# Optimization experiments

Hardware: AMD Instinct MI355X
Metric: run time of the kernel (lower is better)

Reference implementation:

```python
import jax, jax.numpy as jnp
import numpy as np

N = 100000          # nodes
E = 1600000         # edges (before self-loops)
IN = 128
H, C = 4, 32        # heads, out_channels per head
EPS = 1e-5          # BatchNorm eps
NEG_SLOPE = 0.2     # GATConv LeakyReLU slope


def setup_inputs() -> dict:
    key = jax.random.key(0)
    ks = jax.random.split(key, 8)
    return {
        "x": jax.random.normal(ks[0], (N, IN), jnp.float32),
        "edge_index": jax.random.randint(ks[1], (2, E), 0, N, dtype=jnp.int64),
        "W": jax.random.normal(ks[2], (IN, H * C), jnp.float32) * (1.0 / np.sqrt(IN)),
        "att_src": jax.random.normal(ks[3], (H, C), jnp.float32) * 0.1,
        "att_dst": jax.random.normal(ks[4], (H, C), jnp.float32) * 0.1,
        "bias": jax.random.normal(ks[5], (H * C,), jnp.float32) * 0.01,
        "gamma": jnp.ones((H * C,), jnp.float32),
        "beta": jnp.zeros((H * C,), jnp.float32),
    }


def reference(x, edge_index, W, att_src, att_dst, bias, gamma, beta):
    # --- GATConv (concat heads, add self-loops, eval-mode dropout) ---
    loop = jnp.arange(N, dtype=edge_index.dtype)
    src = jnp.concatenate([edge_index[0], loop])  # [E+N] message sources
    dst = jnp.concatenate([edge_index[1], loop])  # [E+N] message targets

    h = (x @ W).reshape(N, H, C)                       # [N,H,C]
    a_s = jnp.einsum('nhc,hc->nh', h, att_src)          # [N,H]
    a_d = jnp.einsum('nhc,hc->nh', h, att_dst)          # [N,H]

    e = a_s[src] + a_d[dst]                             # [E+N,H]
    e = jnp.where(e > 0, e, NEG_SLOPE * e)              # LeakyReLU

    # segment softmax over incoming edges of each dst node
    m = jax.ops.segment_max(e, dst, num_segments=N)     # [N,H]
    ex = jnp.exp(e - m[dst])
    den = jax.ops.segment_sum(ex, dst, num_segments=N)  # [N,H]
    alpha = ex / den[dst]                               # [E+N,H]

    out = jax.ops.segment_sum(h[src] * alpha[:, :, None], dst, num_segments=N)
    out = out.reshape(N, H * C) + bias                  # [N,128]

    # --- ELU activation ---
    out = jax.nn.elu(out)

    # --- BatchNorm1d (training-mode batch statistics, biased variance) ---
    mean = out.mean(axis=0)
    var = out.var(axis=0)
    return (out - mean) * jax.lax.rsqrt(var + EPS) * gamma + beta
```

## Files before the change

### kernel.cpp

```cpp
#include <hip/hip_runtime.h>

#define NEG 0.2f
#define MAXD 128
#define NR 8
#define GEMM_BLOCKS 1024
#define COUNT_BLOCKS 2048

__device__ __forceinline__ float lrelu(float v) { return v > 0.f ? v : NEG * v; }

__device__ __forceinline__ unsigned f2bf(float f) {
  unsigned u = __float_as_uint(f);
  u = (u + 0x7FFFu + ((u >> 16) & 1u)) >> 16;
  return u;
}
__device__ __forceinline__ float bf_lo(unsigned u) { return __uint_as_float(u << 16); }
__device__ __forceinline__ float bf_hi(unsigned u) { return __uint_as_float(u & 0xFFFF0000u); }

typedef __attribute__((ext_vector_type(8))) short bf16x8;
typedef __attribute__((ext_vector_type(4))) float f32x4;

__global__ __launch_bounds__(256) void k_prep(const float* __restrict__ W,
                                              const float* __restrict__ att_src,
                                              const float* __restrict__ att_dst,
                                              unsigned short* __restrict__ Bext) {
  for (int id = blockIdx.x * 256 + threadIdx.x; id < 9 * 4 * 64 * 8; id += gridDim.x * 256) {
    int j = id & 7, lane = (id >> 3) & 63, kb = (id >> 9) & 3, ct = id >> 11;
    int k = kb * 32 + (lane >> 4) * 8 + j;
    int c = ct * 16 + (lane & 15);
    float v;
    if (c < 128) {
      v = W[k * 128 + c];
    } else {
      int slot = c - 128;
      int hd = slot & 3;
      const float* att = (slot < 4) ? att_src : att_dst;
      float s = 0.f;
      for (int jj = 0; jj < 32; ++jj) s = fmaf(W[k * 128 + hd * 32 + jj], att[hd * 32 + jj], s);
      v = s;
    }
    Bext[id] = (unsigned short)f2bf(v);
  }
}

__global__ __launch_bounds__(256) void k_gemm_count(
    const float* __restrict__ x, const unsigned short* __restrict__ Bext,
    unsigned* __restrict__ hb, float* __restrict__ a_s, float* __restrict__ a_d,
    int N, int ntiles,
    const int* __restrict__ ei, int* __restrict__ cnt, int* __restrict__ rank,
    int E, int rsize)
{
  const int tid = threadIdx.x;
  const int chunk = blockIdx.x >> 3;
  if (chunk % 3 == 0) {
    const int vb = (chunk / 3) * 8 + (blockIdx.x & 7);
    const bf16x8* Bfrag = reinterpret_cast<const bf16x8*>(Bext);
    const int w = tid >> 6, lane = tid & 63;
    const int r16 = lane & 15, g = lane >> 4;
    for (int tile = vb; tile < ntiles; tile += GEMM_BLOCKS) {
      int n0 = tile * 64 + w * 16;
      int rowc = min(n0 + r16, N - 1);
      const float* xp = x + (size_t)rowc * 128 + g * 8;
      bf16x8 afr[4];
#pragma unroll
      for (int kb = 0; kb < 4; ++kb) {
        float4 lo = *reinterpret_cast<const float4*>(xp + kb * 32);
        float4 hi = *reinterpret_cast<const float4*>(xp + kb * 32 + 4);
        bf16x8 t;
        t[0] = (short)f2bf(lo.x); t[1] = (short)f2bf(lo.y);
        t[2] = (short)f2bf(lo.z); t[3] = (short)f2bf(lo.w);
        t[4] = (short)f2bf(hi.x); t[5] = (short)f2bf(hi.y);
        t[6] = (short)f2bf(hi.z); t[7] = (short)f2bf(hi.w);
        afr[kb] = t;
      }
#pragma unroll
      for (int ct = 0; ct < 9; ++ct) {
        f32x4 acc = {0.f, 0.f, 0.f, 0.f};
#pragma unroll
        for (int kb = 0; kb < 4; ++kb) {
          bf16x8 bfr = Bfrag[(ct * 4 + kb) * 64 + lane];
          acc = __builtin_amdgcn_mfma_f32_16x16x32_bf16(afr[kb], bfr, acc, 0, 0, 0);
        }
        if (ct < 8) {
#pragma unroll
          for (int r = 0; r < 4; ++r) {
            int orow = n0 + g * 4 + r;
            unsigned b = f2bf(acc[r]);
            unsigned partner = __shfl_xor(b, 1);
            if (((lane & 1) == 0) && orow < N)
              hb[(size_t)orow * 64 + ct * 8 + (r16 >> 1)] = b | (partner << 16);
          }
        } else {
#pragma unroll
          for (int r = 0; r < 4; ++r) {
            int orow = n0 + g * 4 + r;
            if (r16 < 8 && orow < N) {
              if (r16 < 4) a_s[orow * 4 + r16] = acc[r];
              else         a_d[orow * 4 + (r16 - 4)] = acc[r];
            }
          }
        }
      }
    }
  } else {
    const int r = blockIdx.x & 7;
    const int lo = r * rsize, hi = lo + rsize;
    const int cidx = chunk - 1 - (chunk / 3);
    const int gtid = cidx * 256 + tid;
    const int gstride = (COUNT_BLOCKS >> 3) * 256;
    const int nquad = E >> 2;
    const int4* dst4 = reinterpret_cast<const int4*>(ei + E);
    for (int q = gtid; q < nquad; q += gstride) {
      int4 d = dst4[q];
      int e0 = q << 2;
      if (d.x >= lo && d.x < hi) rank[e0]     = atomicAdd(&cnt[d.x], 1);
      if (d.y >= lo && d.y < hi) rank[e0 + 1] = atomicAdd(&cnt[d.y], 1);
      if (d.z >= lo && d.z < hi) rank[e0 + 2] = atomicAdd(&cnt[d.z], 1);
      if (d.w >= lo && d.w < hi) rank[e0 + 3] = atomicAdd(&cnt[d.w], 1);
    }
    for (int e = (nquad << 2) + gtid; e < E; e += gstride) {
      int d = ei[E + e];
      if (d >= lo && d < hi) rank[e] = atomicAdd(&cnt[d], 1);
    }
  }
}

__global__ __launch_bounds__(256) void k_scan1(const int* __restrict__ cnt, int* __restrict__ incl,
                                               int* __restrict__ bsum, int N) {
  __shared__ int sm[256];
  int i = blockIdx.x * 256 + threadIdx.x;
  int v = (i < N) ? cnt[i] : 0;
  sm[threadIdx.x] = v;
  __syncthreads();
  for (int off = 1; off < 256; off <<= 1) {
    int t = (threadIdx.x >= off) ? sm[threadIdx.x - off] : 0;
    __syncthreads();
    sm[threadIdx.x] += t;
    __syncthreads();
  }
  if (i < N) incl[i] = sm[threadIdx.x];
  if (threadIdx.x == 255) bsum[blockIdx.x] = sm[255];
}

__global__ __launch_bounds__(512) void k_scan2(int* __restrict__ bsum, int nb) {
  __shared__ int sm[512];
  int v = (threadIdx.x < nb) ? bsum[threadIdx.x] : 0;
  sm[threadIdx.x] = v;
  __syncthreads();
  for (int off = 1; off < 512; off <<= 1) {
    int t = (threadIdx.x >= off) ? sm[threadIdx.x - off] : 0;
    __syncthreads();
    sm[threadIdx.x] += t;
    __syncthreads();
  }
  if (threadIdx.x < nb) bsum[threadIdx.x] = sm[threadIdx.x];
}

__global__ __launch_bounds__(256) void k_scan3(const int* __restrict__ cnt, const int* __restrict__ incl,
                                               const int* __restrict__ bsum, int* __restrict__ offs,
                                               int N, int E) {
  int i = blockIdx.x * 256 + threadIdx.x;
  if (i < N) {
    int base = (blockIdx.x > 0) ? bsum[blockIdx.x - 1] : 0;
    offs[i] = base + incl[i] - cnt[i];
  }
  if (i == 0) offs[N] = E;
}

__global__ __launch_bounds__(256) void k_scatter_rank(const int* __restrict__ ei,
                                                      const int* __restrict__ offs,
                                                      const int* __restrict__ rank,
                                                      int* __restrict__ ssrc, int E, int rsize) {
  const int r = blockIdx.x & 7;
  const int lo = r * rsize, hi = lo + rsize;
  const int gtid = (blockIdx.x >> 3) * 256 + threadIdx.x;
  const int gstride = (gridDim.x >> 3) * 256;
  const int nquad = E >> 2;
  const int4* dst4 = reinterpret_cast<const int4*>(ei + E);
  for (int q = gtid; q < nquad; q += gstride) {
    int4 d = dst4[q];
    int e0 = q << 2;
    if (d.x >= lo && d.x < hi) ssrc[offs[d.x] + rank[e0]]     = ei[e0];
    if (d.y >= lo && d.y < hi) ssrc[offs[d.y] + rank[e0 + 1]] = ei[e0 + 1];
    if (d.z >= lo && d.z < hi) ssrc[offs[d.z] + rank[e0 + 2]] = ei[e0 + 2];
    if (d.w >= lo && d.w < hi) ssrc[offs[d.w] + rank[e0 + 3]] = ei[e0 + 3];
  }
  for (int e = (nquad << 2) + gtid; e < E; e += gstride) {
    int d = ei[E + e];
    if (d >= lo && d < hi) ssrc[offs[d] + rank[e]] = ei[e];
  }
}

__global__ __launch_bounds__(256) void k_agg(
    const unsigned* __restrict__ hb, const float* __restrict__ a_s, const float* __restrict__ a_d,
    const int* __restrict__ offs, const int* __restrict__ ssrc,
    const float* __restrict__ bias, unsigned* __restrict__ preb,
    float* __restrict__ bnpart, int N)
{
  __shared__ float al[4][MAXD][4];
  __shared__ int   ls[4][MAXD];
  __shared__ float sv[4][128];
  const int wv = threadIdx.x >> 6;
  const int lane = threadIdx.x & 63;
  const int n = blockIdx.x * 4 + wv;

  if (n < N) {
    const int hsel = lane >> 4;
    const int start = offs[n], end = offs[n + 1];
    const int deg = end - start;
    const int jm = deg < MAXD ? deg : MAXD;
    float4 adv = *reinterpret_cast<const float4*>(&a_d[n * 4]);
    float4 asv = *reinterpret_cast<const float4*>(&a_s[n * 4]);
    float e0 = __expf(lrelu(asv.x + adv.x));
    float e1 = __expf(lrelu(asv.y + adv.y));
    float e2 = __expf(lrelu(asv.z + adv.z));
    float e3 = __expf(lrelu(asv.w + adv.w));
    float p0 = 0.f, p1 = 0.f, p2 = 0.f, p3 = 0.f;
    for (int j = lane; j < deg; j += 64) {
      int s = ssrc[start + j];
      float4 av = *reinterpret_cast<const float4*>(&a_s[s * 4]);
      float x0 = __expf(lrelu(av.x + adv.x));
      float x1 = __expf(lrelu(av.y + adv.y));
      float x2 = __expf(lrelu(av.z + adv.z));
      float x3 = __expf(lrelu(av.w + adv.w));
      p0 += x0; p1 += x1; p2 += x2; p3 += x3;
      if (j < MAXD) {
        float4 t = make_float4(x0, x1, x2, x3);
        *reinterpret_cast<float4*>(&al[wv][j][0]) = t;
        ls[wv][j] = s;
      }
    }
#pragma unroll
    for (int off = 32; off >= 1; off >>= 1) {
      p0 += __shfl_xor(p0, off);
      p1 += __shfl_xor(p1, off);
      p2 += __shfl_xor(p2, off);
      p3 += __shfl_xor(p3, off);
    }
    float rden0 = 1.f / (p0 + e0), rden1 = 1.f / (p1 + e1);
    float rden2 = 1.f / (p2 + e2), rden3 = 1.f / (p3 + e3);
    for (int j = lane; j < jm; j += 64) {
      float4 t = *reinterpret_cast<float4*>(&al[wv][j][0]);
      t.x *= rden0; t.y *= rden1; t.z *= rden2; t.w *= rden3;
      *reinterpret_cast<float4*>(&al[wv][j][0]) = t;
    }
    float ad_c = (hsel < 2) ? (hsel == 0 ? adv.x : adv.y) : (hsel == 2 ? adv.z : adv.w);
    float rden = (hsel < 2) ? (hsel == 0 ? rden0 : rden1) : (hsel == 2 ? rden2 : rden3);
    float esf = (hsel < 2) ? (hsel == 0 ? e0 : e1) : (hsel == 2 ? e2 : e3);
    unsigned us = hb[(size_t)n * 64 + lane];
    float wself = esf * rden;
    float acc0 = wself * bf_lo(us);
    float acc1 = wself * bf_hi(us);
    int j = 0;
    for (; j + 8 <= jm; j += 8) {
      int4 sA = *reinterpret_cast<int4*>(&ls[wv][j]);
      int4 sB = *reinterpret_cast<int4*>(&ls[wv][j + 4]);
      unsigned u0 = hb[(size_t)sA.x * 64 + lane];
      unsigned u1 = hb[(size_t)sA.y * 64 + lane];
      unsigned u2 = hb[(size_t)sA.z * 64 + lane];
      unsigned u3 = hb[(size_t)sA.w * 64 + lane];
      unsigned u4 = hb[(size_t)sB.x * 64 + lane];
      unsigned u5 = hb[(size_t)sB.y * 64 + lane];
      unsigned u6 = hb[(size_t)sB.z * 64 + lane];
      unsigned u7 = hb[(size_t)sB.w * 64 + lane];
      float w0 = al[wv][j][hsel];
      float w1 = al[wv][j + 1][hsel];
      float w2 = al[wv][j + 2][hsel];
      float w3 = al[wv][j + 3][hsel];
      float w4 = al[wv][j + 4][hsel];
      float w5 = al[wv][j + 5][hsel];
      float w6 = al[wv][j + 6][hsel];
      float w7 = al[wv][j + 7][hsel];
      acc0 = fmaf(w0, bf_lo(u0), acc0);
      acc1 = fmaf(w0, bf_hi(u0), acc1);
      acc0 = fmaf(w1, bf_lo(u1), acc0);
      acc1 = fmaf(w1, bf_hi(u1), acc1);
      acc0 = fmaf(w2, bf_lo(u2), acc0);
      acc1 = fmaf(w2, bf_hi(u2), acc1);
      acc0 = fmaf(w3, bf_lo(u3), acc0);
      acc1 = fmaf(w3, bf_hi(u3), acc1);
      acc0 = fmaf(w4, bf_lo(u4), acc0);
      acc1 = fmaf(w4, bf_hi(u4), acc1);
      acc0 = fmaf(w5, bf_lo(u5), acc0);
      acc1 = fmaf(w5, bf_hi(u5), acc1);
      acc0 = fmaf(w6, bf_lo(u6), acc0);
      acc1 = fmaf(w6, bf_hi(u6), acc1);
      acc0 = fmaf(w7, bf_lo(u7), acc0);
      acc1 = fmaf(w7, bf_hi(u7), acc1);
    }
    for (; j + 4 <= jm; j += 4) {
      int4 s4 = *reinterpret_cast<int4*>(&ls[wv][j]);
      unsigned u0 = hb[(size_t)s4.x * 64 + lane];
      unsigned u1 = hb[(size_t)s4.y * 64 + lane];
      unsigned u2 = hb[(size_t)s4.z * 64 + lane];
      unsigned u3 = hb[(size_t)s4.w * 64 + lane];
      float w0 = al[wv][j][hsel];
      float w1 = al[wv][j + 1][hsel];
      float w2 = al[wv][j + 2][hsel];
      float w3 = al[wv][j + 3][hsel];
      acc0 = fmaf(w0, bf_lo(u0), acc0);
      acc1 = fmaf(w0, bf_hi(u0), acc1);
      acc0 = fmaf(w1, bf_lo(u1), acc0);
      acc1 = fmaf(w1, bf_hi(u1), acc1);
      acc0 = fmaf(w2, bf_lo(u2), acc0);
      acc1 = fmaf(w2, bf_hi(u2), acc1);
      acc0 = fmaf(w3, bf_lo(u3), acc0);
      acc1 = fmaf(w3, bf_hi(u3), acc1);
    }
    for (; j < jm; ++j) {
      int s = ls[wv][j];
      float w = al[wv][j][hsel];
      unsigned u = hb[(size_t)s * 64 + lane];
      acc0 = fmaf(w, bf_lo(u), acc0);
      acc1 = fmaf(w, bf_hi(u), acc1);
    }
    for (int jj = MAXD; jj < deg; ++jj) {
      int s = ssrc[start + jj];
      float q = a_s[s * 4 + hsel];
      unsigned u = hb[(size_t)s * 64 + lane];
      float w = __expf(lrelu(q + ad_c)) * rden;
      acc0 = fmaf(w, bf_lo(u), acc0);
      acc1 = fmaf(w, bf_hi(u), acc1);
    }
    float2 bv = *reinterpret_cast<const float2*>(&bias[2 * lane]);
    float o0 = acc0 + bv.x;
    float o1 = acc1 + bv.y;
    o0 = o0 > 0.f ? o0 : expm1f(o0);
    o1 = o1 > 0.f ? o1 : expm1f(o1);
    preb[(size_t)n * 64 + lane] = f2bf(o0) | (f2bf(o1) << 16);
    sv[wv][2 * lane] = o0;
    sv[wv][2 * lane + 1] = o1;
  } else {
    sv[wv][2 * lane] = 0.f;
    sv[wv][2 * lane + 1] = 0.f;
  }
  __syncthreads();
  int t = threadIdx.x;
  if (t < 128) {
    float s = 0.f, q = 0.f;
#pragma unroll
    for (int w2 = 0; w2 < 4; ++w2) {
      float v = sv[w2][t];
      s += v;
      q = fmaf(v, v, q);
    }
    float* slot = bnpart + (size_t)(blockIdx.x & 63) * 256;
    atomicAdd(&slot[t], s);
    atomicAdd(&slot[128 + t], q);
  }
}

__global__ void k_bnfinal(const float* __restrict__ bnpart,
                          const float* __restrict__ gamma, const float* __restrict__ beta,
                          float* __restrict__ sc, float* __restrict__ sh, int N) {
  int c = threadIdx.x;
  float s = 0.f, q = 0.f;
  for (int p = 0; p < 64; ++p) {
    s += bnpart[p * 256 + c];
    q += bnpart[p * 256 + 128 + c];
  }
  float invn = 1.f / (float)N;
  float mean = s * invn;
  float var = q * invn - mean * mean;
  float scl = gamma[c] * rsqrtf(var + 1e-5f);
  sc[c] = scl;
  sh[c] = beta[c] - mean * scl;
}

__global__ __launch_bounds__(256) void k_bnapply(const unsigned* __restrict__ preb,
                                                 float* __restrict__ out,
                                                 const float* __restrict__ sc,
                                                 const float* __restrict__ sh, int npair2) {
  int i = blockIdx.x * blockDim.x + threadIdx.x;
  if (i >= npair2) return;
  uint2 u = reinterpret_cast<const uint2*>(preb)[i];
  int p0 = i * 2;
  int c0 = (p0 & 63) * 2;
  float4 scv = *reinterpret_cast<const float4*>(&sc[c0]);
  float4 shv = *reinterpret_cast<const float4*>(&sh[c0]);
  float4 v;
  v.x = fmaf(bf_lo(u.x), scv.x, shv.x);
  v.y = fmaf(bf_hi(u.x), scv.y, shv.y);
  v.z = fmaf(bf_lo(u.y), scv.z, shv.z);
  v.w = fmaf(bf_hi(u.y), scv.w, shv.w);
  reinterpret_cast<float4*>(out)[i] = v;
}

extern "C" void kernel_launch(void* const* d_in, const int* in_sizes, int n_in,
                              void* d_out, int out_size, void* d_ws, size_t ws_size,
                              hipStream_t stream) {
  const float* x = (const float*)d_in[0];
  const int* ei = (const int*)d_in[1];
  const float* W = (const float*)d_in[2];
  const float* att_src = (const float*)d_in[3];
  const float* att_dst = (const float*)d_in[4];
  const float* bias = (const float*)d_in[5];
  const float* gamma = (const float*)d_in[6];
  const float* beta = (const float*)d_in[7];
  float* out = (float*)d_out;

  const int N = in_sizes[0] / 128;
  const int E = in_sizes[1] / 2;

  char* ws = (char*)d_ws;
  size_t off = 0;
  auto alloc = [&](size_t bytes) {
    void* p = ws + off;
    off = (off + bytes + 255) & ~(size_t)255;
    return p;
  };
  unsigned* hb = (unsigned*)alloc((size_t)N * 64 * 4);
  float* a_s = (float*)alloc((size_t)N * 4 * 4);
  float* a_d = (float*)alloc((size_t)N * 4 * 4);
  int* cnt = (int*)alloc((size_t)N * 4);
  int* incl = (int*)alloc((size_t)N * 4);
  int* offs = (int*)alloc((size_t)(N + 1) * 4);
  int* bsum = (int*)alloc(512 * 4);
  int* rank = (int*)alloc((size_t)E * 4);
  int* ssrc = (int*)alloc((size_t)E * 4);
  unsigned* preb = (unsigned*)alloc((size_t)N * 64 * 4);
  float* bnpart = (float*)alloc(64 * 256 * 4);
  float* sc = (float*)alloc(128 * 4);
  float* sh = (float*)alloc(128 * 4);
  unsigned short* Bext = (unsigned short*)alloc(9 * 4 * 64 * 8 * 2);
  (void)n_in; (void)out_size; (void)ws_size;

  hipMemsetAsync(cnt, 0, (size_t)N * 4, stream);
  hipMemsetAsync(bnpart, 0, 64 * 256 * 4, stream);

  k_prep<<<9, 256, 0, stream>>>(W, att_src, att_dst, Bext);

  int ntiles = (N + 63) / 64;
  int rsize = (N + NR - 1) / NR;
  k_gemm_count<<<GEMM_BLOCKS + COUNT_BLOCKS, 256, 0, stream>>>(
      x, Bext, hb, a_s, a_d, N, ntiles, ei, cnt, rank, E, rsize);

  int nb = (N + 255) / 256;
  k_scan1<<<nb, 256, 0, stream>>>(cnt, incl, bsum, N);
  k_scan2<<<1, 512, 0, stream>>>(bsum, nb);
  k_scan3<<<nb, 256, 0, stream>>>(cnt, incl, bsum, offs, N, E);

  k_scatter_rank<<<2048, 256, 0, stream>>>(ei, offs, rank, ssrc, E, rsize);

  k_agg<<<(N + 3) / 4, 256, 0, stream>>>(hb, a_s, a_d, offs, ssrc, bias, preb, bnpart, N);

  k_bnfinal<<<1, 128, 0, stream>>>(bnpart, gamma, beta, sc, sh, N);

  int npair2 = N * 32;
  k_bnapply<<<(npair2 + 255) / 256, 256, 0, stream>>>(preb, out, sc, sh, npair2);
}
```

Measured before the change: 237.7 us.

## Split degree counting into eight private count arrays by edge range

The degree-count phase now gives each of eight block groups a contiguous edge range and its own private count array (reusing the preb buffer). Before, every group read all edges and filtered by destination range. Each edge's destination is now read once, with a vectorized rank store instead of up to four scattered ones. The scan folds the eight per-range counts into per-range prefix offsets, and the scatter adds the matching offset. The cost is an 8N memset and an extra gathered cnt8 read per edge in the scatter, and the private copies may behave differently in L2 than one shared array.

```diff
diff --git a/kernel.cpp b/kernel.cpp
--- a/kernel.cpp
+++ b/kernel.cpp
@@ -2,7 +2,6 @@
 
 #define NEG 0.2f
 #define MAXD 128
-#define NR 8
 #define GEMM_BLOCKS 1024
 #define COUNT_BLOCKS 2048
 
@@ -46,8 +45,8 @@
     const float* __restrict__ x, const unsigned short* __restrict__ Bext,
     unsigned* __restrict__ hb, float* __restrict__ a_s, float* __restrict__ a_d,
     int N, int ntiles,
-    const int* __restrict__ ei, int* __restrict__ cnt, int* __restrict__ rank,
-    int E, int rsize)
+    const int* __restrict__ ei, int* __restrict__ cnt8, int* __restrict__ rank,
+    int E, int esh)
 {
   const int tid = threadIdx.x;
   const int chunk = blockIdx.x >> 3;
@@ -103,33 +102,48 @@
     }
   } else {
     const int r = blockIdx.x & 7;
-    const int lo = r * rsize, hi = lo + rsize;
     const int cidx = chunk - 1 - (chunk / 3);
-    const int gtid = cidx * 256 + tid;
-    const int gstride = (COUNT_BLOCKS >> 3) * 256;
-    const int nquad = E >> 2;
-    const int4* dst4 = reinterpret_cast<const int4*>(ei + E);
-    for (int q = gtid; q < nquad; q += gstride) {
-      int4 d = dst4[q];
-      int e0 = q << 2;
-      if (d.x >= lo && d.x < hi) rank[e0]     = atomicAdd(&cnt[d.x], 1);
-      if (d.y >= lo && d.y < hi) rank[e0 + 1] = atomicAdd(&cnt[d.y], 1);
-      if (d.z >= lo && d.z < hi) rank[e0 + 2] = atomicAdd(&cnt[d.z], 1);
-      if (d.w >= lo && d.w < hi) rank[e0 + 3] = atomicAdd(&cnt[d.w], 1);
-    }
-    for (int e = (nquad << 2) + gtid; e < E; e += gstride) {
-      int d = ei[E + e];
-      if (d >= lo && d < hi) rank[e] = atomicAdd(&cnt[d], 1);
-    }
-  }
-}
-
-__global__ __launch_bounds__(256) void k_scan1(const int* __restrict__ cnt, int* __restrict__ incl,
-                                               int* __restrict__ bsum, int N) {
+    const int qper = 1 << (esh - 2);
+    const int ebase = r << esh;
+    int* cpriv = cnt8 + (size_t)r * N;
+    for (int ql = cidx * 256 + tid; ql < qper; ql += 256 * 256) {
+      int e0 = ebase + (ql << 2);
+      if (e0 >= E) break;
+      if (e0 + 3 < E) {
+        int4 d = *reinterpret_cast<const int4*>(ei + E + e0);
+        int4 rk;
+        rk.x = atomicAdd(&cpriv[d.x], 1);
+        rk.y = atomicAdd(&cpriv[d.y], 1);
+        rk.z = atomicAdd(&cpriv[d.z], 1);
+        rk.w = atomicAdd(&cpriv[d.w], 1);
+        *reinterpret_cast<int4*>(rank + e0) = rk;
+      } else {
+        for (int e = e0; e < E; ++e) {
+          int d = ei[E + e];
+          rank[e] = atomicAdd(&cpriv[d], 1);
+        }
+      }
+    }
+  }
+}
+
+__global__ __launch_bounds__(256) void k_scan1(int* __restrict__ cnt8, int* __restrict__ cnt,
+                                               int* __restrict__ incl, int* __restrict__ bsum, int N) {
   __shared__ int sm[256];
   int i = blockIdx.x * 256 + threadIdx.x;
-  int v = (i < N) ? cnt[i] : 0;
-  sm[threadIdx.x] = v;
+  int tot = 0;
+  if (i < N) {
+    int run = 0;
+#pragma unroll
+    for (int r = 0; r < 8; ++r) {
+      int t = cnt8[(size_t)r * N + i];
+      cnt8[(size_t)r * N + i] = run;
+      run += t;
+    }
+    cnt[i] = run;
+    tot = run;
+  }
+  sm[threadIdx.x] = tot;
   __syncthreads();
   for (int off = 1; off < 256; off <<= 1) {
     int t = (threadIdx.x >= off) ? sm[threadIdx.x - off] : 0;
@@ -168,8 +182,10 @@
 
 __global__ __launch_bounds__(256) void k_scatter_rank(const int* __restrict__ ei,
                                                       const int* __restrict__ offs,
+                                                      const int* __restrict__ cnt8,
                                                       const int* __restrict__ rank,
-                                                      int* __restrict__ ssrc, int E, int rsize) {
+                                                      int* __restrict__ ssrc, int E, int rsize,
+                                                      int esh, int N) {
   const int r = blockIdx.x & 7;
   const int lo = r * rsize, hi = lo + rsize;
   const int gtid = (blockIdx.x >> 3) * 256 + threadIdx.x;
@@ -179,14 +195,14 @@
   for (int q = gtid; q < nquad; q += gstride) {
     int4 d = dst4[q];
     int e0 = q << 2;
-    if (d.x >= lo && d.x < hi) ssrc[offs[d.x] + rank[e0]]     = ei[e0];
-    if (d.y >= lo && d.y < hi) ssrc[offs[d.y] + rank[e0 + 1]] = ei[e0 + 1];
-    if (d.z >= lo && d.z < hi) ssrc[offs[d.z] + rank[e0 + 2]] = ei[e0 + 2];
-    if (d.w >= lo && d.w < hi) ssrc[offs[d.w] + rank[e0 + 3]] = ei[e0 + 3];
+    if (d.x >= lo && d.x < hi) ssrc[offs[d.x] + cnt8[(size_t)(e0 >> esh) * N + d.x] + rank[e0]]         = ei[e0];
+    if (d.y >= lo && d.y < hi) ssrc[offs[d.y] + cnt8[(size_t)((e0+1) >> esh) * N + d.y] + rank[e0 + 1]] = ei[e0 + 1];
+    if (d.z >= lo && d.z < hi) ssrc[offs[d.z] + cnt8[(size_t)((e0+2) >> esh) * N + d.z] + rank[e0 + 2]] = ei[e0 + 2];
+    if (d.w >= lo && d.w < hi) ssrc[offs[d.w] + cnt8[(size_t)((e0+3) >> esh) * N + d.w] + rank[e0 + 3]] = ei[e0 + 3];
   }
   for (int e = (nquad << 2) + gtid; e < E; e += gstride) {
     int d = ei[E + e];
-    if (d >= lo && d < hi) ssrc[offs[d] + rank[e]] = ei[e];
+    if (d >= lo && d < hi) ssrc[offs[d] + cnt8[(size_t)(e >> esh) * N + d] + rank[e]] = ei[e];
   }
 }
 
@@ -424,22 +440,27 @@
   unsigned short* Bext = (unsigned short*)alloc(9 * 4 * 64 * 8 * 2);
   (void)n_in; (void)out_size; (void)ws_size;
 
-  hipMemsetAsync(cnt, 0, (size_t)N * 4, stream);
+  int* cnt8 = (int*)preb;
+
+  int esh = 10;
+  while (((E + (1 << esh) - 1) >> esh) > 8) ++esh;
+
+  hipMemsetAsync(cnt8, 0, (size_t)N * 8 * 4, stream);
   hipMemsetAsync(bnpart, 0, 64 * 256 * 4, stream);
 
   k_prep<<<9, 256, 0, stream>>>(W, att_src, att_dst, Bext);
 
   int ntiles = (N + 63) / 64;
-  int rsize = (N + NR - 1) / NR;
   k_gemm_count<<<GEMM_BLOCKS + COUNT_BLOCKS, 256, 0, stream>>>(
-      x, Bext, hb, a_s, a_d, N, ntiles, ei, cnt, rank, E, rsize);
+      x, Bext, hb, a_s, a_d, N, ntiles, ei, cnt8, rank, E, esh);
 
   int nb = (N + 255) / 256;
-  k_scan1<<<nb, 256, 0, stream>>>(cnt, incl, bsum, N);
+  k_scan1<<<nb, 256, 0, stream>>>(cnt8, cnt, incl, bsum, N);
   k_scan2<<<1, 512, 0, stream>>>(bsum, nb);
   k_scan3<<<nb, 256, 0, stream>>>(cnt, incl, bsum, offs, N, E);
 
-  k_scatter_rank<<<2048, 256, 0, stream>>>(ei, offs, rank, ssrc, E, rsize);
+  int rsize = (N + 7) / 8;
+  k_scatter_rank<<<2048, 256, 0, stream>>>(ei, offs, cnt8, rank, ssrc, E, rsize, esh, N);
 
   k_agg<<<(N + 3) / 4, 256, 0, stream>>>(hb, a_s, a_d, offs, ssrc, bias, preb, bnpart, N);
 
```

Result: no change. 234.0 us (-1.6%).
